# Kernel tuning notes

Hardware: AMD Instinct MI355X
Metric: run time of the kernel (lower is better)

## Reference

```python
import jax, jax.numpy as jnp
import numpy as np

UNITS = 128
D_FEAT = 128
B, N = 4, 4096
EDGE_PROB = 0.01  # avg in-degree ~ N * EDGE_PROB ~ 41


def setup_inputs() -> dict:
    key = jax.random.key(0)
    k1, k2, k3, k4 = jax.random.split(key, 4)
    x = jax.random.normal(k1, (B, N, D_FEAT), dtype=jnp.float32)
    # binary adjacency mask, as consumed by tf.where(adj)
    adj = (jax.random.uniform(k2, (B, N, N)) < EDGE_PROB).astype(jnp.float32)
    # Dense(units, use_bias=False) kernels: msg on concat(x_snd, x_rec) -> [2d, U];
    # node_update on concat(x, messages) -> [d+U, U]
    W_msg = (jax.random.normal(k3, (2 * D_FEAT, UNITS), dtype=jnp.float32)
             / np.sqrt(2 * D_FEAT).astype(np.float32))
    W_upd = (jax.random.normal(k4, (D_FEAT + UNITS, UNITS), dtype=jnp.float32)
             / np.sqrt(D_FEAT + UNITS).astype(np.float32))
    return {"x": x, "adj": adj, "W_msg": W_msg, "W_upd": W_upd}


def reference(x, adj, W_msg, W_upd):
    # Faithful to MPNN2.call: edges are (b, s, r) where adj[b, s, r] != 0.
    # message per edge = concat(x[b,s], x[b,r]) @ W_msg = x[b,s]@Ws + x[b,r]@Wr.
    # messages[b,r] = segment_mean over incoming edges. Since the receiver term
    # x[b,r]@Wr is identical for all edges into r, its mean is itself, and the
    # sender term's mean is (adj^T @ (x@Ws)) / in_degree. Empty segments -> 0
    # (tf.math.unsorted_segment_mean semantics). This avoids data-dependent
    # edge-list shapes and is jit-compatible.
    d = x.shape[-1]
    Ws, Wr = W_msg[:d], W_msg[d:]          # [d, U] each
    xs = x @ Ws                            # sender contribution  [B, N, U]
    xr = x @ Wr                            # receiver contribution [B, N, U]
    deg = jnp.einsum('bsr->br', adj)[..., None]          # in-degree [B, N, 1]
    snd_sum = jnp.einsum('bsr,bsu->bru', adj, xs)        # [B, N, U]
    messages = jnp.where(deg > 0,
                         snd_sum / jnp.maximum(deg, 1.0) + xr,
                         0.0)
    # node_update on concat(x, messages); activation=None, use_bias=False
    return jnp.concatenate([x, messages], axis=-1) @ W_upd
```

## Files before the change

kernel.cpp:

```cpp
#include <hip/hip_runtime.h>
#include <hip/hip_bf16.h>

#define BB 4
#define NN 4096
#define ROWS (BB*NN)
#define RT 256
#define SC 512
#define NCH (NN/SC)
#define CAPC 32
#define BSTRIDE (NCH*CAPC)

__device__ __forceinline__ float asf(unsigned int u) {
    union { unsigned int i; float f; } cv; cv.i = u; return cv.f;
}
__device__ __forceinline__ unsigned short f2bf(float f) {
    union { float f; unsigned int i; } cv; cv.f = f;
    unsigned int i = cv.i;
    return (unsigned short)((i + 0x7FFFu + ((i >> 16) & 1u)) >> 16);
}

__global__ __launch_bounds__(256) void scan_bucket(const float* __restrict__ adj,
                                                   int* __restrict__ cnt2,
                                                   int* __restrict__ bucket) {
    __shared__ int lcnt[RT];
    int bI = blockIdx.x;
    int rt = bI & 15;
    int ch = (bI >> 4) & 7;
    int b  = bI >> 7;
    int r0 = rt * RT;
    int s0 = ch * SC;
    int t  = threadIdx.x;
    lcnt[t] = 0;
    __syncthreads();
    int cg = t & 63;
    int sl = t >> 6;
    const float* base = adj + ((size_t)b * NN + s0) * NN + r0 + cg * 4;
    for (int k = 0; k < SC / 4; ++k) {
        int srow = k * 4 + sl;
        float4 v = *(const float4*)(base + (size_t)srow * NN);
        int s = s0 + srow;
        float vals[4] = {v.x, v.y, v.z, v.w};
#pragma unroll
        for (int j = 0; j < 4; ++j) {
            if (vals[j] != 0.0f) {
                int col = cg * 4 + j;
                int slot = atomicAdd(&lcnt[col], 1);
                if (slot < CAPC)
                    bucket[(size_t)((b << 12) + r0 + col) * BSTRIDE + ch * CAPC + slot] = s;
            }
        }
    }
    __syncthreads();
    cnt2[(size_t)((b << 12) + r0 + t) * NCH + ch] = lcnt[t];
}

__global__ __launch_bounds__(128) void fold_weights(const float* __restrict__ Wmsg,
                                                    const float* __restrict__ Wupd,
                                                    float* __restrict__ Wcat) {
    __shared__ float ldsS[128], ldsR[128];
    int k = blockIdx.x, t = threadIdx.x;
    ldsS[t] = Wmsg[k * 128 + t];
    ldsR[t] = Wmsg[(128 + k) * 128 + t];
    __syncthreads();
    float a1 = 0.f, a2 = 0.f;
#pragma unroll 8
    for (int m = 0; m < 128; ++m) {
        float wu = Wupd[(128 + m) * 128 + t];
        a1 += ldsS[m] * wu;
        a2 += ldsR[m] * wu;
    }
    Wcat[k * 384 + t]       = Wupd[k * 128 + t];
    Wcat[k * 384 + 128 + t] = a2;
    Wcat[k * 384 + 256 + t] = a1;
}

#define BM 64
#define BK 64
#define BN 128
__global__ __launch_bounds__(256) void gemm_x_wcat(const float* __restrict__ X,
                                                   const float* __restrict__ Wcat,
                                                   float* __restrict__ TD,
                                                   unsigned short* __restrict__ YB) {
    __shared__ float As[BM][68];
    __shared__ float Bs[BK][BN];
    int t  = threadIdx.x;
    int m0 = blockIdx.x * BM;
    int nb = blockIdx.y;
    int n0 = nb * BN;
    int cn = t & 15;
    int cm = t >> 4;

    float acc[4][8];
#pragma unroll
    for (int i = 0; i < 4; ++i)
#pragma unroll
        for (int j = 0; j < 8; ++j) acc[i][j] = 0.f;

    for (int c = 0; c < 2; ++c) {
#pragma unroll
        for (int i = 0; i < 4; ++i) {
            int f = t + 256 * i;
            int m = f >> 4, k4 = f & 15;
            float4 v = *(const float4*)(X + (size_t)(m0 + m) * 128 + c * 64 + k4 * 4);
            *(float4*)(&As[m][k4 * 4]) = v;
        }
#pragma unroll
        for (int i = 0; i < 8; ++i) {
            int f = t + 256 * i;
            int k = f >> 5, n4 = f & 31;
            float4 v = *(const float4*)(Wcat + (size_t)(c * 64 + k) * 384 + n0 + n4 * 4);
            *(float4*)(&Bs[k][n4 * 4]) = v;
        }
        __syncthreads();
#pragma unroll 8
        for (int kk = 0; kk < BK; ++kk) {
            float av[4];
#pragma unroll
            for (int i = 0; i < 4; ++i) av[i] = As[cm * 4 + i][kk];
            float4 b0 = *(float4*)(&Bs[kk][cn * 8]);
            float4 b1 = *(float4*)(&Bs[kk][cn * 8 + 4]);
            float bv[8] = {b0.x, b0.y, b0.z, b0.w, b1.x, b1.y, b1.z, b1.w};
#pragma unroll
            for (int i = 0; i < 4; ++i)
#pragma unroll
                for (int j = 0; j < 8; ++j) acc[i][j] += av[i] * bv[j];
        }
        __syncthreads();
    }
#pragma unroll
    for (int i = 0; i < 4; ++i) {
        int row = m0 + cm * 4 + i;
        if (nb == 2) {
            uint4 o;
            o.x = (unsigned)f2bf(acc[i][0]) | ((unsigned)f2bf(acc[i][1]) << 16);
            o.y = (unsigned)f2bf(acc[i][2]) | ((unsigned)f2bf(acc[i][3]) << 16);
            o.z = (unsigned)f2bf(acc[i][4]) | ((unsigned)f2bf(acc[i][5]) << 16);
            o.w = (unsigned)f2bf(acc[i][6]) | ((unsigned)f2bf(acc[i][7]) << 16);
            *(uint4*)(YB + (size_t)row * 128 + cn * 8) = o;
        } else {
            float* dst = TD + (size_t)row * 256 + nb * 128 + cn * 8;
            float4 o0 = {acc[i][0], acc[i][1], acc[i][2], acc[i][3]};
            float4 o1 = {acc[i][4], acc[i][5], acc[i][6], acc[i][7]};
            *(float4*)(dst)     = o0;
            *(float4*)(dst + 4) = o1;
        }
    }
}

__global__ __launch_bounds__(256) void gather_out(const float* __restrict__ TD,
                                                  const unsigned int* __restrict__ YB,
                                                  const int* __restrict__ cnt2,
                                                  const int* __restrict__ bucket,
                                                  float* __restrict__ out) {
    __shared__ int lds_s[4][BSTRIDE];
    int t  = threadIdx.x;
    int rs = t >> 6;
    int j2 = t & 63;
    int rg = blockIdx.x * 4 + rs;

    int c[NCH];
    int ctot = 0, deg = 0;
    int pre[NCH];
#pragma unroll
    for (int ch = 0; ch < NCH; ++ch) {
        c[ch] = cnt2[(size_t)rg * NCH + ch];
        deg += c[ch];
        int cc = min(c[ch], CAPC);
        pre[ch] = ctot;
        ctot += cc;
    }
#pragma unroll
    for (int ch = 0; ch < NCH; ++ch) {
        int cc = min(c[ch], CAPC);
        if (j2 < cc)
            lds_s[rs][pre[ch] + j2] = bucket[(size_t)rg * BSTRIDE + ch * CAPC + j2];
    }
    __syncthreads();

    const float2* td = (const float2*)(TD + (size_t)rg * 256);
    float2 t1 = td[j2];
    float2 res = t1;
    if (deg > 0) {
        int b = rg >> 12;
        const unsigned int* yb = YB + (((size_t)b << 12)) * 64 + j2;
        float al0 = 0.f, ah0 = 0.f, al1 = 0.f, ah1 = 0.f;
        float al2 = 0.f, ah2 = 0.f, al3 = 0.f, ah3 = 0.f;
        int e = 0;
        for (; e + 4 <= ctot; e += 4) {
            int s0 = lds_s[rs][e + 0];
            int s1 = lds_s[rs][e + 1];
            int s2 = lds_s[rs][e + 2];
            int s3 = lds_s[rs][e + 3];
            unsigned u0 = yb[(size_t)s0 * 64];
            unsigned u1 = yb[(size_t)s1 * 64];
            unsigned u2 = yb[(size_t)s2 * 64];
            unsigned u3 = yb[(size_t)s3 * 64];
            al0 += asf(u0 << 16); ah0 += asf(u0 & 0xffff0000u);
            al1 += asf(u1 << 16); ah1 += asf(u1 & 0xffff0000u);
            al2 += asf(u2 << 16); ah2 += asf(u2 & 0xffff0000u);
            al3 += asf(u3 << 16); ah3 += asf(u3 & 0xffff0000u);
        }
        for (; e < ctot; ++e) {
            unsigned u = yb[(size_t)lds_s[rs][e] * 64];
            al0 += asf(u << 16); ah0 += asf(u & 0xffff0000u);
        }
        float inv = 1.0f / (float)deg;
        float2 d2 = td[64 + j2];
        res.x = t1.x + d2.x + (al0 + al1 + al2 + al3) * inv;
        res.y = t1.y + d2.y + (ah0 + ah1 + ah2 + ah3) * inv;
    }
    ((float2*)(out + (size_t)rg * 128))[j2] = res;
}

extern "C" void kernel_launch(void* const* d_in, const int* in_sizes, int n_in,
                              void* d_out, int out_size, void* d_ws, size_t ws_size,
                              hipStream_t stream) {
    const float* x    = (const float*)d_in[0];
    const float* adj  = (const float*)d_in[1];
    const float* Wmsg = (const float*)d_in[2];
    const float* Wupd = (const float*)d_in[3];
    float* out = (float*)d_out;

    char* ws = (char*)d_ws;
    float*          Wcat   = (float*)(ws);
    float*          TD     = (float*)(ws + 262144);
    unsigned short* YB     = (unsigned short*)(ws + 262144 + 16777216);
    int*            cnt2   = (int*)(ws + 262144 + 16777216 + 4194304);
    int*            bucket = (int*)(ws + 262144 + 16777216 + 4194304 + 524288);

    scan_bucket<<<512, 256, 0, stream>>>(adj, cnt2, bucket);
    fold_weights<<<128, 128, 0, stream>>>(Wmsg, Wupd, Wcat);
    gemm_x_wcat<<<dim3(ROWS / BM, 3), 256, 0, stream>>>(x, Wcat, TD, YB);
    gather_out<<<ROWS / 4, 256, 0, stream>>>(TD, (const unsigned int*)YB, cnt2, bucket, out);
}
```

Baseline: 462.8 us.

## Use bf16 MFMA for projection GEMM and widen adjacency scan parallelism

Replaces the fp32 FMA tiled GEMM with a bf16 MFMA kernel: folded weights are stored transposed in bf16 and X is converted to bf16 while staged in LDS. The adjacency scan now uses 128-column tiles with twice as many blocks, and each thread issues four float4 loads before processing them, to raise memory-level parallelism on the dominant 268MB adjacency read. The bf16 inputs lower the precision of the TD outputs, which were fp32 before.

```diff
diff --git a/kernel.cpp b/kernel.cpp
--- a/kernel.cpp
+++ b/kernel.cpp
@@ -4,11 +4,14 @@
 #define BB 4
 #define NN 4096
 #define ROWS (BB*NN)
-#define RT 256
+#define RT 128
 #define SC 512
 #define NCH (NN/SC)
 #define CAPC 32
 #define BSTRIDE (NCH*CAPC)
+
+typedef __attribute__((ext_vector_type(8))) short short8;
+typedef __attribute__((ext_vector_type(4))) float f32x4;
 
 __device__ __forceinline__ float asf(unsigned int u) {
     union { unsigned int i; float f; } cv; cv.i = u; return cv.f;
@@ -24,39 +27,44 @@
                                                    int* __restrict__ bucket) {
     __shared__ int lcnt[RT];
     int bI = blockIdx.x;
-    int rt = bI & 15;
-    int ch = (bI >> 4) & 7;
-    int b  = bI >> 7;
+    int rt = bI & 31;
+    int ch = (bI >> 5) & 7;
+    int b  = bI >> 8;
     int r0 = rt * RT;
     int s0 = ch * SC;
     int t  = threadIdx.x;
-    lcnt[t] = 0;
-    __syncthreads();
-    int cg = t & 63;
-    int sl = t >> 6;
+    if (t < RT) lcnt[t] = 0;
+    __syncthreads();
+    int cg = t & 31;
+    int sl = t >> 5;
     const float* base = adj + ((size_t)b * NN + s0) * NN + r0 + cg * 4;
-    for (int k = 0; k < SC / 4; ++k) {
-        int srow = k * 4 + sl;
-        float4 v = *(const float4*)(base + (size_t)srow * NN);
-        int s = s0 + srow;
-        float vals[4] = {v.x, v.y, v.z, v.w};
-#pragma unroll
-        for (int j = 0; j < 4; ++j) {
-            if (vals[j] != 0.0f) {
-                int col = cg * 4 + j;
-                int slot = atomicAdd(&lcnt[col], 1);
-                if (slot < CAPC)
-                    bucket[(size_t)((b << 12) + r0 + col) * BSTRIDE + ch * CAPC + slot] = s;
+    for (int k = 0; k < SC / 32; ++k) {
+        float4 v[4];
+#pragma unroll
+        for (int u = 0; u < 4; ++u)
+            v[u] = *(const float4*)(base + (size_t)(k * 32 + u * 8 + sl) * NN);
+#pragma unroll
+        for (int u = 0; u < 4; ++u) {
+            int s = s0 + k * 32 + u * 8 + sl;
+            float vals[4] = {v[u].x, v[u].y, v[u].z, v[u].w};
+#pragma unroll
+            for (int j = 0; j < 4; ++j) {
+                if (vals[j] != 0.0f) {
+                    int col = cg * 4 + j;
+                    int slot = atomicAdd(&lcnt[col], 1);
+                    if (slot < CAPC)
+                        bucket[(size_t)((b << 12) + r0 + col) * BSTRIDE + ch * CAPC + slot] = s;
+                }
             }
         }
     }
     __syncthreads();
-    cnt2[(size_t)((b << 12) + r0 + t) * NCH + ch] = lcnt[t];
+    if (t < RT) cnt2[(size_t)((b << 12) + r0 + t) * NCH + ch] = lcnt[t];
 }
 
 __global__ __launch_bounds__(128) void fold_weights(const float* __restrict__ Wmsg,
                                                     const float* __restrict__ Wupd,
-                                                    float* __restrict__ Wcat) {
+                                                    unsigned short* __restrict__ WcatT) {
     __shared__ float ldsS[128], ldsR[128];
     int k = blockIdx.x, t = threadIdx.x;
     ldsS[t] = Wmsg[k * 128 + t];
@@ -69,81 +77,76 @@
         a1 += ldsS[m] * wu;
         a2 += ldsR[m] * wu;
     }
-    Wcat[k * 384 + t]       = Wupd[k * 128 + t];
-    Wcat[k * 384 + 128 + t] = a2;
-    Wcat[k * 384 + 256 + t] = a1;
-}
-
-#define BM 64
-#define BK 64
-#define BN 128
-__global__ __launch_bounds__(256) void gemm_x_wcat(const float* __restrict__ X,
-                                                   const float* __restrict__ Wcat,
-                                                   float* __restrict__ TD,
-                                                   unsigned short* __restrict__ YB) {
-    __shared__ float As[BM][68];
-    __shared__ float Bs[BK][BN];
+    WcatT[(size_t)t * 128 + k]         = f2bf(Wupd[k * 128 + t]);
+    WcatT[(size_t)(128 + t) * 128 + k] = f2bf(a2);
+    WcatT[(size_t)(256 + t) * 128 + k] = f2bf(a1);
+}
+
+__global__ __launch_bounds__(256) void gemm_mfma(const float* __restrict__ X,
+                                                 const unsigned short* __restrict__ WcatT,
+                                                 float* __restrict__ TD,
+                                                 unsigned short* __restrict__ YB) {
+    __shared__ unsigned short Al[64][136];
+    __shared__ unsigned short Bl[128][136];
     int t  = threadIdx.x;
-    int m0 = blockIdx.x * BM;
+    int m0 = blockIdx.x * 64;
     int nb = blockIdx.y;
-    int n0 = nb * BN;
-    int cn = t & 15;
-    int cm = t >> 4;
-
-    float acc[4][8];
-#pragma unroll
-    for (int i = 0; i < 4; ++i)
-#pragma unroll
-        for (int j = 0; j < 8; ++j) acc[i][j] = 0.f;
-
-    for (int c = 0; c < 2; ++c) {
-#pragma unroll
-        for (int i = 0; i < 4; ++i) {
-            int f = t + 256 * i;
-            int m = f >> 4, k4 = f & 15;
-            float4 v = *(const float4*)(X + (size_t)(m0 + m) * 128 + c * 64 + k4 * 4);
-            *(float4*)(&As[m][k4 * 4]) = v;
-        }
+
+    {
+        int m = t >> 2, seg = t & 3;
+        const float* src = X + (size_t)(m0 + m) * 128 + seg * 32;
 #pragma unroll
         for (int i = 0; i < 8; ++i) {
-            int f = t + 256 * i;
-            int k = f >> 5, n4 = f & 31;
-            float4 v = *(const float4*)(Wcat + (size_t)(c * 64 + k) * 384 + n0 + n4 * 4);
-            *(float4*)(&Bs[k][n4 * 4]) = v;
-        }
-        __syncthreads();
-#pragma unroll 8
-        for (int kk = 0; kk < BK; ++kk) {
-            float av[4];
-#pragma unroll
-            for (int i = 0; i < 4; ++i) av[i] = As[cm * 4 + i][kk];
-            float4 b0 = *(float4*)(&Bs[kk][cn * 8]);
-            float4 b1 = *(float4*)(&Bs[kk][cn * 8 + 4]);
-            float bv[8] = {b0.x, b0.y, b0.z, b0.w, b1.x, b1.y, b1.z, b1.w};
-#pragma unroll
-            for (int i = 0; i < 4; ++i)
-#pragma unroll
-                for (int j = 0; j < 8; ++j) acc[i][j] += av[i] * bv[j];
-        }
-        __syncthreads();
-    }
-#pragma unroll
-    for (int i = 0; i < 4; ++i) {
-        int row = m0 + cm * 4 + i;
-        if (nb == 2) {
-            uint4 o;
-            o.x = (unsigned)f2bf(acc[i][0]) | ((unsigned)f2bf(acc[i][1]) << 16);
-            o.y = (unsigned)f2bf(acc[i][2]) | ((unsigned)f2bf(acc[i][3]) << 16);
-            o.z = (unsigned)f2bf(acc[i][4]) | ((unsigned)f2bf(acc[i][5]) << 16);
-            o.w = (unsigned)f2bf(acc[i][6]) | ((unsigned)f2bf(acc[i][7]) << 16);
-            *(uint4*)(YB + (size_t)row * 128 + cn * 8) = o;
-        } else {
-            float* dst = TD + (size_t)row * 256 + nb * 128 + cn * 8;
-            float4 o0 = {acc[i][0], acc[i][1], acc[i][2], acc[i][3]};
-            float4 o1 = {acc[i][4], acc[i][5], acc[i][6], acc[i][7]};
-            *(float4*)(dst)     = o0;
-            *(float4*)(dst + 4) = o1;
-        }
+            float4 v = *(const float4*)(src + i * 4);
+            ushort4 p;
+            p.x = f2bf(v.x); p.y = f2bf(v.y); p.z = f2bf(v.z); p.w = f2bf(v.w);
+            *(ushort4*)&Al[m][seg * 32 + i * 4] = p;
+        }
+    }
+    {
+        int n = t >> 1, half = t & 1;
+        const unsigned short* src = WcatT + (size_t)(nb * 128 + n) * 128 + half * 64;
+#pragma unroll
+        for (int i = 0; i < 8; ++i) {
+            uint4 v = *(const uint4*)(src + i * 8);
+            *(uint4*)&Bl[n][half * 64 + i * 8] = v;
+        }
+    }
+    __syncthreads();
+
+    int lane = t & 63, wave = t >> 6;
+    int quad = lane >> 4, lr = lane & 15;
+    int wm = wave * 16;
+    f32x4 acc[8];
+#pragma unroll
+    for (int s = 0; s < 8; ++s) acc[s] = (f32x4)0.f;
+
+#pragma unroll
+    for (int kk = 0; kk < 4; ++kk) {
+        short8 a = *(short8*)&Al[wm + lr][kk * 32 + quad * 8];
+#pragma unroll
+        for (int s = 0; s < 8; ++s) {
+            short8 bf = *(short8*)&Bl[s * 16 + lr][kk * 32 + quad * 8];
+            acc[s] = __builtin_amdgcn_mfma_f32_16x16x32_bf16(a, bf, acc[s], 0, 0, 0);
+        }
+    }
+
+    if (nb == 2) {
+#pragma unroll
+        for (int s = 0; s < 8; ++s)
+#pragma unroll
+            for (int r = 0; r < 4; ++r) {
+                int row = m0 + wm + quad * 4 + r;
+                YB[(size_t)row * 128 + s * 16 + lr] = f2bf(acc[s][r]);
+            }
+    } else {
+#pragma unroll
+        for (int s = 0; s < 8; ++s)
+#pragma unroll
+            for (int r = 0; r < 4; ++r) {
+                int row = m0 + wm + quad * 4 + r;
+                TD[(size_t)row * 256 + nb * 128 + s * 16 + lr] = acc[s][r];
+            }
     }
 }
 
@@ -222,14 +225,14 @@
     float* out = (float*)d_out;
 
     char* ws = (char*)d_ws;
-    float*          Wcat   = (float*)(ws);
-    float*          TD     = (float*)(ws + 262144);
-    unsigned short* YB     = (unsigned short*)(ws + 262144 + 16777216);
-    int*            cnt2   = (int*)(ws + 262144 + 16777216 + 4194304);
-    int*            bucket = (int*)(ws + 262144 + 16777216 + 4194304 + 524288);
-
-    scan_bucket<<<512, 256, 0, stream>>>(adj, cnt2, bucket);
-    fold_weights<<<128, 128, 0, stream>>>(Wmsg, Wupd, Wcat);
-    gemm_x_wcat<<<dim3(ROWS / BM, 3), 256, 0, stream>>>(x, Wcat, TD, YB);
+    unsigned short* WcatT  = (unsigned short*)(ws);
+    float*          TD     = (float*)(ws + 131072);
+    unsigned short* YB     = (unsigned short*)(ws + 131072 + 16777216);
+    int*            cnt2   = (int*)(ws + 131072 + 16777216 + 4194304);
+    int*            bucket = (int*)(ws + 131072 + 16777216 + 4194304 + 524288);
+
+    scan_bucket<<<1024, 256, 0, stream>>>(adj, cnt2, bucket);
+    fold_weights<<<128, 128, 0, stream>>>(Wmsg, Wupd, WcatT);
+    gemm_mfma<<<dim3(256, 3), 256, 0, stream>>>(x, WcatT, TD, YB);
     gather_out<<<ROWS / 4, 256, 0, stream>>>(TD, (const unsigned int*)YB, cnt2, bucket, out);
 }
```

Measured after the change: 433.2 us. 6.4% less time.
